# Kernel tuning notes

Hardware: AMD Instinct MI355X
Metric: run time of the kernel (lower is better)

Reference implementation:

```python
import jax, jax.numpy as jnp
import numpy as np

DIM, HEADS, WS, SHIFT, HID = 256, 8, 7, 3, 1024
N = WS * WS

def _rel_index():
    coords = np.stack(np.meshgrid(np.arange(WS), np.arange(WS), indexing='ij')).reshape(2, -1)
    rel = (coords[:, :, None] - coords[:, None, :]).transpose(1, 2, 0)
    rel[:, :, 0] += WS - 1
    rel[:, :, 1] += WS - 1
    rel[:, :, 0] *= 2 * WS - 1
    return rel.sum(-1)  # [N, N] int

def _attn_mask(hp, wp):
    img = np.zeros((hp, wp))
    slices = (slice(0, -WS), slice(-WS, -SHIFT), slice(-SHIFT, None))
    cnt = 0
    for hs in slices:
        for ws_ in slices:
            img[hs, ws_] = cnt
            cnt += 1
    mw = img.reshape(hp // WS, WS, wp // WS, WS).transpose(0, 2, 1, 3).reshape(-1, N)
    am = mw[:, None, :] - mw[:, :, None]  # [nw, N, N]
    return np.where(am != 0, -100.0, 0.0).astype(np.float32)

def _ln(t, g, b):
    mu = t.mean(-1, keepdims=True)
    var = ((t - mu) ** 2).mean(-1, keepdims=True)
    return (t - mu) / jnp.sqrt(var + 1e-5) * g + b

def setup_inputs() -> dict:
    key = jax.random.key(0)
    ks = jax.random.split(key, 16)
    b, h, w = 16, 112, 112
    p = lambda k, shape: jax.random.normal(k, shape, dtype=jnp.float32) * 0.02
    return {
        'x': jax.random.normal(ks[0], (b, h * w, DIM), dtype=jnp.float32),
        'norm1_w': jnp.ones((DIM,), jnp.float32), 'norm1_b': jnp.zeros((DIM,), jnp.float32),
        'qkv_w': p(ks[1], (DIM, 3 * DIM)), 'qkv_b': jnp.zeros((3 * DIM,), jnp.float32),
        'proj_w': p(ks[2], (DIM, DIM)), 'proj_b': jnp.zeros((DIM,), jnp.float32),
        'bias_table': p(ks[3], ((2 * WS - 1) * (2 * WS - 1), HEADS)),
        'norm2_w': jnp.ones((DIM,), jnp.float32), 'norm2_b': jnp.zeros((DIM,), jnp.float32),
        'fc1_w': p(ks[4], (DIM, HID)), 'fc1_b': jnp.zeros((HID,), jnp.float32),
        'fc2_w': p(ks[5], (HID, DIM)), 'fc2_b': jnp.zeros((DIM,), jnp.float32),
        'h': h, 'w': w,
    }

def reference(x, norm1_w, norm1_b, qkv_w, qkv_b, proj_w, proj_b, bias_table,
              norm2_w, norm2_b, fc1_w, fc1_b, fc2_w, fc2_b, h, w):
    b, l, c = x.shape
    hd = c // HEADS
    shortcut = x
    xn = _ln(x, norm1_w, norm1_b).reshape(b, h, w, c)
    pad_b, pad_r = (-h) % WS, (-w) % WS
    if pad_b or pad_r:
        xn = jnp.pad(xn, ((0, 0), (0, pad_b), (0, pad_r), (0, 0)))
    hp, wp = h + pad_b, w + pad_r
    xs = jnp.roll(xn, (-SHIFT, -SHIFT), (1, 2))
    # window partition -> [B_, N, c]
    win = xs.reshape(b, hp // WS, WS, wp // WS, WS, c).transpose(0, 1, 3, 2, 4, 5).reshape(-1, N, c)
    qkv = (win @ qkv_w + qkv_b).reshape(-1, N, 3, HEADS, hd).transpose(2, 0, 3, 1, 4)
    q, k, v = qkv[0] * (hd ** -0.5), qkv[1], qkv[2]
    attn = jnp.einsum('bhnd,bhmd->bhnm', q, k)  # [B_, H, N, N]
    rpb = bias_table[jnp.asarray(_rel_index().reshape(-1))].reshape(N, N, HEADS).transpose(2, 0, 1)
    attn = attn + rpb[None]
    mask = jnp.asarray(_attn_mask(hp, wp))  # [nw, N, N]
    nw = mask.shape[0]
    attn = (attn.reshape(b, nw, HEADS, N, N) + mask[None, :, None]).reshape(-1, HEADS, N, N)
    attn = jax.nn.softmax(attn, axis=-1)
    out = jnp.einsum('bhnm,bhmd->bhnd', attn, v).transpose(0, 2, 1, 3).reshape(-1, N, c)
    out = out @ proj_w + proj_b
    # window reverse
    out = out.reshape(b, hp // WS, wp // WS, WS, WS, c).transpose(0, 1, 3, 2, 4, 5).reshape(b, hp, wp, c)
    out = jnp.roll(out, (SHIFT, SHIFT), (1, 2))[:, :h, :w].reshape(b, h * w, c)
    x = shortcut + out
    x = x + (jax.nn.gelu(_ln(x, norm2_w, norm2_b) @ fc1_w + fc1_b, approximate=False) @ fc2_w + fc2_b)
    return x
```

## Files before the change

### kernel.cpp

```cpp
#include <hip/hip_runtime.h>
#include <stdint.h>
#include <math.h>

#define DIMC   256
#define NHEADS 8
#define WSZ    7
#define NTOK   49
#define HIDN   1024
#define IMGS   112
#define BATCH  16
#define NWIN   4096
#define MTOT   200704

using frag_ab = __attribute__((ext_vector_type(8))) short;
using frag_cd = __attribute__((ext_vector_type(4))) float;

__device__ __forceinline__ float b2f(ushort u) {
    union { float f; uint32_t i; } c; c.i = ((uint32_t)u) << 16; return c.f;
}
__device__ __forceinline__ ushort f2b(float f) {
    union { float f; uint32_t i; } c; c.f = f;
    uint32_t r = c.i + 0x7fffu + ((c.i >> 16) & 1u);
    return (ushort)(r >> 16);
}

__device__ __forceinline__ void gld16(const ushort* g, ushort* l) {
    __builtin_amdgcn_global_load_lds(
        (const __attribute__((address_space(1))) void*)g,
        (__attribute__((address_space(3))) void*)l, 16, 0, 0);
}

__global__ void detect_kernel(const uint32_t* __restrict__ w, int* __restrict__ flag) {
    if (threadIdx.x == 0 && blockIdx.x == 0)
        *flag = (w[0] == 0x3F800000u) ? 1 : 0;
}

__global__ void cvt_kernel(const void* __restrict__ src, ushort* __restrict__ dst,
                           int n, const int* __restrict__ dflag) {
    int i = blockIdx.x * 256 + threadIdx.x;
    if (i < n)
        dst[i] = (*dflag) ? f2b(((const float*)src)[i]) : ((const ushort*)src)[i];
}

__global__ void transpose_cvt(const void* __restrict__ src, ushort* __restrict__ dst,
                              int K, int N, const int* __restrict__ dflag) {
    int idx = blockIdx.x * 256 + threadIdx.x;
    if (idx < K * N) {
        int k = idx / N, n = idx - k * N;
        ushort v = (*dflag) ? f2b(((const float*)src)[idx]) : ((const ushort*)src)[idx];
        dst[n * K + k] = v;
    }
}

template <bool REMAP>
__global__ __launch_bounds__(256)
void ln_kernel(const void* __restrict__ xin, const ushort* __restrict__ g,
               const ushort* __restrict__ bt, ushort* __restrict__ out,
               const int* __restrict__ dflag) {
    int gw = (blockIdx.x * 256 + threadIdx.x) >> 6;
    int lane = threadIdx.x & 63;
    if (gw >= MTOT) return;
    float v0, v1, v2, v3;
    if constexpr (REMAP) {
        if (*dflag) {
            float4 xv = *(const float4*)((const float*)xin + (size_t)gw * DIMC + lane * 4);
            v0 = xv.x; v1 = xv.y; v2 = xv.z; v3 = xv.w;
        } else {
            ushort4 xv = *(const ushort4*)((const ushort*)xin + (size_t)gw * DIMC + lane * 4);
            v0 = b2f(xv.x); v1 = b2f(xv.y); v2 = b2f(xv.z); v3 = b2f(xv.w);
        }
    } else {
        ushort4 xv = *(const ushort4*)((const ushort*)xin + (size_t)gw * DIMC + lane * 4);
        v0 = b2f(xv.x); v1 = b2f(xv.y); v2 = b2f(xv.z); v3 = b2f(xv.w);
    }
    float s = v0 + v1 + v2 + v3;
#pragma unroll
    for (int off = 32; off; off >>= 1) s += __shfl_xor(s, off);
    float mean = s * (1.f / 256.f);
    float d0 = v0 - mean, d1 = v1 - mean, d2 = v2 - mean, d3 = v3 - mean;
    float q = d0 * d0 + d1 * d1 + d2 * d2 + d3 * d3;
#pragma unroll
    for (int off = 32; off; off >>= 1) q += __shfl_xor(q, off);
    float inv = rsqrtf(q * (1.f / 256.f) + 1e-5f);
    ushort4 gv = *(const ushort4*)(g + lane * 4);
    ushort4 bv = *(const ushort4*)(bt + lane * 4);
    ushort4 o;
    o.x = f2b(d0 * inv * b2f(gv.x) + b2f(bv.x));
    o.y = f2b(d1 * inv * b2f(gv.y) + b2f(bv.y));
    o.z = f2b(d2 * inv * b2f(gv.z) + b2f(bv.z));
    o.w = f2b(d3 * inv * b2f(gv.w) + b2f(bv.w));
    size_t orow;
    if constexpr (REMAP) {
        int b = gw / 12544, sres = gw - b * 12544;
        int row = sres / IMGS, col = sres - row * IMGS;
        int r = row - 3; if (r < 0) r += IMGS;
        int c = col - 3; if (c < 0) c += IMGS;
        int wh = r / WSZ, tr = r - wh * WSZ;
        int ww = c / WSZ, tc = c - ww * WSZ;
        orow = (size_t)(((b * 16 + wh) * 16 + ww)) * NTOK + (tr * WSZ + tc);
    } else {
        orow = gw;
    }
    *(ushort4*)(out + orow * DIMC + lane * 4) = o;
}

template <int MODE>
__global__ __launch_bounds__(256)
void gemm_bt(const ushort* __restrict__ A, const ushort* __restrict__ Bt,
             const ushort* __restrict__ bias, void* __restrict__ outv,
             const void* __restrict__ add, int M, int N, int K,
             const int* __restrict__ dflag, int nbn) {
    __shared__ __align__(16) ushort As[2][128 * 32];
    __shared__ __align__(16) ushort Bs[2][128 * 32];
    const int t = threadIdx.x;
    const int lane = t & 63, wave = t >> 6;
    const int wr = (wave >> 1) * 64, wc = (wave & 1) * 64;
    const int lrow = lane & 15, lq8 = (lane >> 4) * 8;
    const int lid = blockIdx.x;
    const int xcd = lid & 7, idx = lid >> 3;
    const int ppx = (M >> 7) >> 3;
    const int bn = (idx % nbn) * 128;
    const int bm = (xcd * ppx + idx / nbn) * 128;
    const int arow = t >> 2, acol = (t & 3) * 8;

    int isf32 = 0;
    if constexpr (MODE == 1) isf32 = *dflag;

    frag_cd acc[4][4];
#pragma unroll
    for (int i = 0; i < 4; i++)
#pragma unroll
        for (int j = 0; j < 4; j++) acc[i][j] = (frag_cd){0.f, 0.f, 0.f, 0.f};

    const ushort* Ag0 = A + (size_t)(bm + arow) * K + acol;
    const ushort* Ag1 = Ag0 + (size_t)64 * K;
    const ushort* Bg0 = Bt + (size_t)(bn + arow) * K + acol;
    const ushort* Bg1 = Bg0 + (size_t)64 * K;
    const int lofs0 = arow * 32 + acol;
    const int lofs1 = (arow + 64) * 32 + acol;

    gld16(Ag0, &As[0][lofs0]);
    gld16(Ag1, &As[0][lofs1]);
    gld16(Bg0, &Bs[0][lofs0]);
    gld16(Bg1, &Bs[0][lofs1]);
    __syncthreads();

    int cur = 0;
    for (int kk = 0; kk < K; kk += 32) {
        const int nxt = cur ^ 1;
        if (kk + 32 < K) {
            gld16(Ag0 + kk + 32, &As[nxt][lofs0]);
            gld16(Ag1 + kk + 32, &As[nxt][lofs1]);
            gld16(Bg0 + kk + 32, &Bs[nxt][lofs0]);
            gld16(Bg1 + kk + 32, &Bs[nxt][lofs1]);
        }
        frag_ab af[4], bfr[4];
#pragma unroll
        for (int i = 0; i < 4; i++)
            af[i] = *(const frag_ab*)&As[cur][(wr + i * 16 + lrow) * 32 + lq8];
#pragma unroll
        for (int j = 0; j < 4; j++)
            bfr[j] = *(const frag_ab*)&Bs[cur][(wc + j * 16 + lrow) * 32 + lq8];
#pragma unroll
        for (int i = 0; i < 4; i++)
#pragma unroll
            for (int j = 0; j < 4; j++)
                acc[i][j] = __builtin_amdgcn_mfma_f32_16x16x32_bf16(
                    af[i], bfr[j], acc[i][j], 0, 0, 0);
        __syncthreads();
        cur = nxt;
    }

    ushort* out = (ushort*)outv;
    float*  outf = (float*)outv;

#pragma unroll
    for (int i = 0; i < 4; i++) {
#pragma unroll
        for (int rg = 0; rg < 4; rg++) {
            const int gm = bm + wr + i * 16 + (lane >> 4) * 4 + rg;
            int win = 0, tok = 0;
            size_t rowbase = 0;
            if constexpr (MODE == 0) {
                win = gm / 49; tok = gm - win * 49;
            } else if constexpr (MODE == 1) {
                win = gm / 49; tok = gm - win * 49;
                int b = win >> 8, wh = (win >> 4) & 15, ww = win & 15;
                int tr = tok / 7, tc = tok - tr * 7;
                int r = wh * 7 + tr + 3; if (r >= IMGS) r -= IMGS;
                int c = ww * 7 + tc + 3; if (c >= IMGS) c -= IMGS;
                rowbase = ((size_t)b * 12544 + r * IMGS + c) * DIMC;
            } else {
                rowbase = (size_t)gm * N;
            }
#pragma unroll
            for (int j = 0; j < 4; j++) {
                const int gn = bn + wc + j * 16 + lrow;
                float v = acc[i][j][rg] + b2f(bias[gn]);
                if constexpr (MODE == 0) {
                    int part = gn >> 8, hd = (gn >> 5) & 7, dd = gn & 31;
                    if (part == 0) v *= 0.17677669529663687f;
                    out[(size_t)part * ((size_t)MTOT * DIMC) +
                        (((size_t)win * NHEADS + hd) * NTOK + tok) * 32 + dd] = f2b(v);
                } else if constexpr (MODE == 1) {
                    float r = isf32 ? ((const float*)add)[rowbase + gn]
                                    : b2f(((const ushort*)add)[rowbase + gn]);
                    v += r;
                    out[rowbase + gn] = f2b(v);
                } else if constexpr (MODE == 2) {
                    v = 0.5f * v * (1.f + erff(v * 0.70710678118654752f));
                    out[rowbase + gn] = f2b(v);
                } else {
                    v += b2f(((const ushort*)add)[rowbase + gn]);
                    outf[rowbase + gn] = v;
                }
            }
        }
    }
}

__global__ __launch_bounds__(256)
void attn_kernel(const ushort* __restrict__ qb, const ushort* __restrict__ kb,
                 const ushort* __restrict__ vb, const ushort* __restrict__ btab,
                 ushort* __restrict__ out) {
    __shared__ __align__(16) ushort Pl[4][2][16][72];
    __shared__ __align__(16) ushort Vl[4][32][72];
    __shared__ float bbs[4][172];
    const int t = threadIdx.x;
    const int wv = t >> 6, l = t & 63;
    const int lo = l & 15, hi = l >> 4;
    const int gw = blockIdx.x * 4 + wv;
    const int win = gw >> 3, hd = gw & 7;
    const int wh = (win >> 4) & 15, ww = win & 15;

    for (int idx = l; idx < 169; idx += 64)
        bbs[wv][idx] = b2f(btab[idx * NHEADS + hd]);

    const ushort* qp = qb + (size_t)gw * (NTOK * 32);
    const ushort* kp = kb + (size_t)gw * (NTOK * 32);
    const ushort* vp = vb + (size_t)gw * (NTOK * 32);

    frag_ab vreg[4];
#pragma unroll
    for (int q = 0; q < 4; q++) {
        if (l < NTOK)
            vreg[q] = *(const frag_ab*)(vp + l * 32 + q * 8);
        else
            vreg[q] = (frag_ab){0, 0, 0, 0, 0, 0, 0, 0};
    }

    frag_ab af[4], bfr[4];
#pragma unroll
    for (int i = 0; i < 4; i++) {
        af[i]  = *(const frag_ab*)(qp + (i * 16 + lo) * 32 + hi * 8);
        bfr[i] = *(const frag_ab*)(kp + (i * 16 + lo) * 32 + hi * 8);
    }
    frag_cd S[4][4];
#pragma unroll
    for (int i = 0; i < 4; i++)
#pragma unroll
        for (int j = 0; j < 4; j++) S[i][j] = (frag_cd){0.f, 0.f, 0.f, 0.f};
#pragma unroll
    for (int i = 0; i < 4; i++)
#pragma unroll
        for (int j = 0; j < 4; j++)
            S[i][j] = __builtin_amdgcn_mfma_f32_16x16x32_bf16(af[i], bfr[j], S[i][j], 0, 0, 0);

#pragma unroll
    for (int q = 0; q < 4; q++)
#pragma unroll
        for (int e = 0; e < 8; e++)
            Vl[wv][q * 8 + e][l] = (ushort)vreg[q][e];
    frag_ab vf[2][2];
#pragma unroll
    for (int j = 0; j < 2; j++)
#pragma unroll
        for (int kk = 0; kk < 2; kk++)
            vf[j][kk] = *(const frag_ab*)&Vl[wv][j * 16 + lo][kk * 32 + hi * 8];

    int cy[4], cx[4], rvj[4], rhj[4];
#pragma unroll
    for (int j = 0; j < 4; j++) {
        int c = j * 16 + lo;
        int y = (c * 9363) >> 16;
        cy[j] = y; cx[j] = c - y * 7;
        rvj[j] = (wh < 15) ? 0 : ((cy[j] < 4) ? 1 : 2);
        rhj[j] = (ww < 15) ? 0 : ((cx[j] < 4) ? 1 : 2);
    }

    frag_cd o[4][2];
#pragma unroll
    for (int i = 0; i < 4; i++)
#pragma unroll
        for (int j = 0; j < 2; j++) o[i][j] = (frag_cd){0.f, 0.f, 0.f, 0.f};

#pragma unroll
    for (int i = 0; i < 4; i++) {
        const int cur = i & 1;
#pragma unroll
        for (int rg = 0; rg < 4; rg++) {
            int r = i * 16 + hi * 4 + rg;
            int rr = (r < NTOK) ? r : 0;
            int yi = (rr * 9363) >> 16, xi = rr - yi * 7;
            int rvi = (wh < 15) ? 0 : ((yi < 4) ? 1 : 2);
            int rhi = (ww < 15) ? 0 : ((xi < 4) ? 1 : 2);
            float xs[4];
#pragma unroll
            for (int j = 0; j < 4; j++) {
                bool valid = (j < 3) | (lo == 0);
                float v = S[i][j][rg]
                        + bbs[wv][(yi - cy[j] + 6) * 13 + (xi - cx[j] + 6)];
                v = (rvi != rvj[j] || rhi != rhj[j]) ? v - 100.f : v;
                xs[j] = valid ? v : -1e30f;
            }
            float m = fmaxf(fmaxf(xs[0], xs[1]), fmaxf(xs[2], xs[3]));
#pragma unroll
            for (int off = 8; off; off >>= 1) m = fmaxf(m, __shfl_xor(m, off));
            float e0 = __expf(xs[0] - m);
            float e1 = __expf(xs[1] - m);
            float e2 = __expf(xs[2] - m);
            float e3 = __expf(xs[3] - m);
            float sum = e0 + e1 + e2 + e3;
#pragma unroll
            for (int off = 8; off; off >>= 1) sum += __shfl_xor(sum, off);
            float inv = 1.f / sum;
            int rl = hi * 4 + rg;
            int sw = ((rl >> 3) & 1) << 4;
            ushort* prow = &Pl[wv][cur][rl][0];
            prow[(lo +  0) ^ sw] = f2b(e0 * inv);
            prow[(lo + 16) ^ sw] = f2b(e1 * inv);
            prow[(lo + 32) ^ sw] = f2b(e2 * inv);
            prow[(lo + 48) ^ sw] = f2b(e3 * inv);
        }
        int swr = ((lo >> 3) & 1) << 4;
        frag_ab pa0 = *(const frag_ab*)&Pl[wv][cur][lo][(      hi * 8) ^ swr];
        frag_ab pa1 = *(const frag_ab*)&Pl[wv][cur][lo][(32 + hi * 8) ^ swr];
#pragma unroll
        for (int j = 0; j < 2; j++) {
            o[i][j] = __builtin_amdgcn_mfma_f32_16x16x32_bf16(pa0, vf[j][0], o[i][j], 0, 0, 0);
            o[i][j] = __builtin_amdgcn_mfma_f32_16x16x32_bf16(pa1, vf[j][1], o[i][j], 0, 0, 0);
        }
    }

#pragma unroll
    for (int i = 0; i < 4; i++)
#pragma unroll
        for (int rg = 0; rg < 4; rg++) {
            int r = i * 16 + hi * 4 + rg;
            if (r < NTOK) {
                size_t ob = ((size_t)win * NTOK + r) * DIMC + hd * 32;
                out[ob + lo]      = f2b(o[i][0][rg]);
                out[ob + 16 + lo] = f2b(o[i][1][rg]);
            }
        }
}

extern "C" void kernel_launch(void* const* d_in, const int* in_sizes, int n_in,
                              void* d_out, int out_size, void* d_ws, size_t ws_size,
                              hipStream_t stream) {
    (void)in_sizes; (void)n_in; (void)out_size;
    const void* x        = d_in[0];
    const void* norm1_w  = d_in[1];
    const void* norm1_b  = d_in[2];
    const void* qkv_w    = d_in[3];
    const void* qkv_b    = d_in[4];
    const void* proj_w   = d_in[5];
    const void* proj_b   = d_in[6];
    const void* btab     = d_in[7];
    const void* norm2_w  = d_in[8];
    const void* norm2_b  = d_in[9];
    const void* fc1_w    = d_in[10];
    const void* fc1_b    = d_in[11];
    const void* fc2_w    = d_in[12];
    const void* fc2_b    = d_in[13];

    const size_t szA   = (size_t)MTOT * DIMC * 2;
    const size_t szBIG = (size_t)MTOT * HIDN * 2;
    const size_t szWT  = (size_t)(768 * 256 + 256 * 256 + 256 * 1024 + 1024 * 256) * 2;
    const size_t szSV  = 16384;
    const size_t need  = szSV + szA * 2 + szBIG + szWT;
    if (ws_size < need) return;

    char* ws = (char*)d_ws;
    ushort* sv    = (ushort*)ws;
    ushort* svN1w = sv + 0;
    ushort* svN1b = sv + 256;
    ushort* svQKb = sv + 512;
    ushort* svPJb = sv + 1280;
    ushort* svN2w = sv + 1536;
    ushort* svN2b = sv + 1792;
    ushort* svF1b = sv + 2048;
    ushort* svF2b = sv + 3072;
    ushort* svBT  = sv + 3328;
    int*    dflag = (int*)(ws + szSV - 256);

    char* big = ws + szSV;
    ushort* bufA   = (ushort*)big;
    ushort* bufBIG = (ushort*)(big + szA);
    ushort* bufQ   = bufBIG;
    ushort* bufK   = bufBIG + (size_t)MTOT * DIMC;
    ushort* bufV   = bufBIG + (size_t)2 * MTOT * DIMC;
    ushort* bufX1  = (ushort*)(big + szA + szBIG);
    ushort* qkvT   = (ushort*)(big + szA + szBIG + szA);
    ushort* projT  = qkvT + 768 * 256;
    ushort* fc1T   = projT + 256 * 256;
    ushort* fc2T   = fc1T + 256 * 1024;

    detect_kernel<<<1, 64, 0, stream>>>((const uint32_t*)norm1_w, dflag);

    cvt_kernel<<<1, 256, 0, stream>>>(norm1_w, svN1w, 256, dflag);
    cvt_kernel<<<1, 256, 0, stream>>>(norm1_b, svN1b, 256, dflag);
    cvt_kernel<<<3, 256, 0, stream>>>(qkv_b,  svQKb, 768, dflag);
    cvt_kernel<<<1, 256, 0, stream>>>(proj_b, svPJb, 256, dflag);
    cvt_kernel<<<1, 256, 0, stream>>>(norm2_w, svN2w, 256, dflag);
    cvt_kernel<<<1, 256, 0, stream>>>(norm2_b, svN2b, 256, dflag);
    cvt_kernel<<<4, 256, 0, stream>>>(fc1_b,  svF1b, 1024, dflag);
    cvt_kernel<<<1, 256, 0, stream>>>(fc2_b,  svF2b, 256, dflag);
    cvt_kernel<<<6, 256, 0, stream>>>(btab,   svBT, 1352, dflag);

    transpose_cvt<<<(768 * 256 + 255) / 256, 256, 0, stream>>>(qkv_w, qkvT, 256, 768, dflag);
    transpose_cvt<<<(256 * 256 + 255) / 256, 256, 0, stream>>>(proj_w, projT, 256, 256, dflag);
    transpose_cvt<<<(256 * 1024 + 255) / 256, 256, 0, stream>>>(fc1_w, fc1T, 256, 1024, dflag);
    transpose_cvt<<<(1024 * 256 + 255) / 256, 256, 0, stream>>>(fc2_w, fc2T, 1024, 256, dflag);

    ln_kernel<true><<<MTOT / 4, 256, 0, stream>>>(x, svN1w, svN1b, bufA, dflag);

    gemm_bt<0><<<6 * (MTOT / 128), 256, 0, stream>>>(
        bufA, qkvT, svQKb, bufBIG, nullptr, MTOT, 768, 256, dflag, 6);

    attn_kernel<<<NWIN * NHEADS / 4, 256, 0, stream>>>(bufQ, bufK, bufV, svBT, bufA);

    gemm_bt<1><<<2 * (MTOT / 128), 256, 0, stream>>>(
        bufA, projT, svPJb, bufX1, x, MTOT, 256, 256, dflag, 2);

    ln_kernel<false><<<MTOT / 4, 256, 0, stream>>>(bufX1, svN2w, svN2b, bufA, dflag);

    gemm_bt<2><<<8 * (MTOT / 128), 256, 0, stream>>>(
        bufA, fc1T, svF1b, bufBIG, nullptr, MTOT, 1024, 256, dflag, 8);

    gemm_bt<3><<<2 * (MTOT / 128), 256, 0, stream>>>(
        bufBIG, fc2T, svF2b, d_out, bufX1, MTOT, 256, 1024, dflag, 2);
}
```

Measured before the change: 1.462 ms.

## Triple-buffer GEMM LDS tiles with vmcnt waits and approximate erf in GELU

The bf16 GEMM main loop moves from double buffering with __syncthreads to a three-stage LDS ring. Loads are issued two tiles ahead, and explicit s_waitcnt vmcnt counts plus s_barrier let outstanding global loads overlap the MFMAs. Separately, the exact erff in the fc1 GELU epilogue becomes the Abramowitz-Stegun polynomial using rcp and exp. The ring costs more LDS per block, which may lower occupancy, and the GELU result now has about 1e-7 absolute error, well within bf16 output precision.

```diff
diff --git a/kernel.cpp b/kernel.cpp
--- a/kernel.cpp
+++ b/kernel.cpp
@@ -110,8 +110,8 @@
              const ushort* __restrict__ bias, void* __restrict__ outv,
              const void* __restrict__ add, int M, int N, int K,
              const int* __restrict__ dflag, int nbn) {
-    __shared__ __align__(16) ushort As[2][128 * 32];
-    __shared__ __align__(16) ushort Bs[2][128 * 32];
+    __shared__ __align__(16) ushort As[3][128 * 32];
+    __shared__ __align__(16) ushort Bs[3][128 * 32];
     const int t = threadIdx.x;
     const int lane = t & 63, wave = t >> 6;
     const int wr = (wave >> 1) * 64, wc = (wave & 1) * 64;
@@ -139,21 +139,33 @@
     const int lofs0 = arow * 32 + acol;
     const int lofs1 = (arow + 64) * 32 + acol;
 
-    gld16(Ag0, &As[0][lofs0]);
-    gld16(Ag1, &As[0][lofs1]);
-    gld16(Bg0, &Bs[0][lofs0]);
-    gld16(Bg1, &Bs[0][lofs1]);
-    __syncthreads();
-
-    int cur = 0;
-    for (int kk = 0; kk < K; kk += 32) {
-        const int nxt = cur ^ 1;
-        if (kk + 32 < K) {
-            gld16(Ag0 + kk + 32, &As[nxt][lofs0]);
-            gld16(Ag1 + kk + 32, &As[nxt][lofs1]);
-            gld16(Bg0 + kk + 32, &Bs[nxt][lofs0]);
-            gld16(Bg1 + kk + 32, &Bs[nxt][lofs1]);
-        }
+    const int nt = K >> 5;
+    gld16(Ag0,      &As[0][lofs0]);
+    gld16(Ag1,      &As[0][lofs1]);
+    gld16(Bg0,      &Bs[0][lofs0]);
+    gld16(Bg1,      &Bs[0][lofs1]);
+    gld16(Ag0 + 32, &As[1][lofs0]);
+    gld16(Ag1 + 32, &As[1][lofs1]);
+    gld16(Bg0 + 32, &Bs[1][lofs0]);
+    gld16(Bg1 + 32, &Bs[1][lofs1]);
+
+    int cur = 0, st = 2, kpre = 64;
+    for (int tt = 0; tt < nt; ++tt) {
+        asm volatile("s_barrier" ::: "memory");
+        if (tt + 2 < nt) {
+            gld16(Ag0 + kpre, &As[st][lofs0]);
+            gld16(Ag1 + kpre, &As[st][lofs1]);
+            gld16(Bg0 + kpre, &Bs[st][lofs0]);
+            gld16(Bg1 + kpre, &Bs[st][lofs1]);
+            kpre += 32;
+            asm volatile("s_waitcnt vmcnt(8)" ::: "memory");
+        } else if (tt + 1 < nt) {
+            asm volatile("s_waitcnt vmcnt(4)" ::: "memory");
+        } else {
+            asm volatile("s_waitcnt vmcnt(0)" ::: "memory");
+        }
+        asm volatile("s_barrier" ::: "memory");
+
         frag_ab af[4], bfr[4];
 #pragma unroll
         for (int i = 0; i < 4; i++)
@@ -167,8 +179,8 @@
             for (int j = 0; j < 4; j++)
                 acc[i][j] = __builtin_amdgcn_mfma_f32_16x16x32_bf16(
                     af[i], bfr[j], acc[i][j], 0, 0, 0);
-        __syncthreads();
-        cur = nxt;
+        cur = (cur == 2) ? 0 : cur + 1;
+        st  = (st == 2) ? 0 : st + 1;
     }
 
     ushort* out = (ushort*)outv;
@@ -208,7 +220,14 @@
                     v += r;
                     out[rowbase + gn] = f2b(v);
                 } else if constexpr (MODE == 2) {
-                    v = 0.5f * v * (1.f + erff(v * 0.70710678118654752f));
+                    float a  = fabsf(v) * 0.70710678118654752f;
+                    float rc = __builtin_amdgcn_rcpf(1.f + 0.3275911f * a);
+                    float p  = rc * (0.254829592f + rc * (-0.284496736f +
+                               rc * (1.421413741f + rc * (-1.453152027f +
+                               rc * 1.061405429f))));
+                    float er = 1.f - p * __expf(-a * a);
+                    er = (v < 0.f) ? -er : er;
+                    v = 0.5f * v * (1.f + er);
                     out[rowbase + gn] = f2b(v);
                 } else {
                     v += b2f(((const ushort*)add)[rowbase + gn]);
```

Result: slower. 1.523 ms (+4.1%).
